# Kernel optimization log

Hardware: AMD Instinct MI355X
Metric: run time of the kernel (lower is better)

Reference implementation:

```python
import jax, jax.numpy as jnp
import numpy as np

ALPHA = 2000.0
TAU = 1e-07
K = 3
TOL = 1e-06
MAX_ITER = 50
T = 1048576  # 2**20
EPS = 1e-08


def setup_inputs() -> dict:
    key = jax.random.key(0)
    k1, k2 = jax.random.split(key)
    x = jax.random.normal(k1, (T,), dtype=jnp.float32)
    omega0 = jax.random.uniform(k2, (K,), dtype=jnp.float32)  # torch does 0.5*rand(K); scaled in reference
    return {"x": x, "omega0": omega0}


def _vmd(x, omega0):
    Tn = x.shape[0]
    freqs = jnp.arange(1, Tn + 1, dtype=jnp.float32) / Tn - 0.5 - 1.0 / Tn  # [T]
    f_hat = jnp.fft.fftshift(jnp.fft.fft(x.astype(jnp.complex64)))  # [T] complex64
    omega = 0.5 * omega0  # init == 1
    u0 = jnp.zeros((K, Tn), dtype=jnp.complex64)
    lam0 = jnp.zeros((Tn,), dtype=jnp.complex64)

    def step(carry, n):
        u_out, u_prev, lam_prev, om, done = carry
        # --- u_hat update (vectorized over k; torch k-loop uses stale omega) ---
        d_self = (freqs[None, :] - om[:, None]) ** 2            # [K,T]
        denom = d_self + TAU ** 2
        denom = denom.at[1:].add(d_self[:-1])                    # + (freqs - omega[k-1])^2 for k>0
        denom = denom.at[:-1].add(d_self[1:])                    # + (freqs - omega[k+1])^2 for k<K-1
        u_new = (f_hat[None, :] - lam_prev[None, :] / 2) / (1.0 + ALPHA * denom)  # [K,T]
        # --- omega update (DC == 0 branch) ---
        power = jnp.abs(u_new) ** 2                              # [K,T] float32
        om_new = jnp.sum(power * freqs[None, :], axis=1) / (jnp.sum(power, axis=1) + EPS)
        # --- dual ascent ---
        lam_new = lam_prev + TAU * (jnp.sum(u_new, axis=0) - f_hat)
        # --- convergence check every 10 outer iterations (torch break -> done flag) ---
        u_diff = jnp.sum(jnp.abs(u_new - u_prev) ** 2) / (jnp.sum(jnp.abs(u_prev) ** 2) + EPS)
        o_diff = jnp.sum(jnp.abs(om_new - jnp.roll(om_new, 1))) / K
        conv = (n % 10 == 0) & (u_diff < TOL) & (o_diff < TOL)
        new = (u_new, u_new, lam_new, om_new, done | conv)
        old = (u_out, u_prev, lam_prev, om, done)
        out = jax.tree_util.tree_map(lambda a, b: jnp.where(done, a, b), old, new)
        return out, None

    carry = (u0, u0, lam0, omega, jnp.array(False))
    (u_final, _, _, _, _), _ = jax.lax.scan(step, carry, jnp.arange(MAX_ITER))
    imfs = jnp.fft.ifft(jnp.fft.ifftshift(u_final, axes=1), axis=1).real.astype(x.dtype)  # [K,T]
    return imfs


def reference(x, omega0):
    return _vmd(x, omega0)
```

## Files before the change

### kernel.cpp

```cpp
#include <hip/hip_runtime.h>
#include <math.h>


#define TN        (1 << 20)
#define NBINS     1024
#define PPB       1024
#define FALPHA    2000.0f
#define FTAU      1e-7f
#define FTOL      1e-6f
#define FEPS      1e-8f
#define FTWO_PI   6.28318530717958647692f
#define FINV_T    (1.0f / 1048576.0f)

__device__ __forceinline__ float2 cmulf(float2 a, float2 b) {
    return make_float2(a.x * b.x - a.y * b.y, a.x * b.y + a.y * b.x);
}
__device__ __forceinline__ float2 cisf(float a) {
    float s, c;
    __sincosf(a, &s, &c);
    return make_float2(c, s);
}
__device__ __forceinline__ float rlanef(float v, int l) {
    return __int_as_float(__builtin_amdgcn_readlane(__float_as_int(v), l));
}

__device__ __forceinline__ void g3f(float fr, float om0, float om1, float om2,
                                    float& g0, float& g1, float& g2) {
    const float tau2 = FTAU * FTAU;
    float d0 = fr - om0; d0 *= d0;
    float d1 = fr - om1; d1 *= d1;
    float d2 = fr - om2; d2 *= d2;
    g0 = __builtin_amdgcn_rcpf(1.0f + FALPHA * (d0 + d1 + tau2));
    g1 = __builtin_amdgcn_rcpf(1.0f + FALPHA * (d0 + d1 + d2 + tau2));
    g2 = __builtin_amdgcn_rcpf(1.0f + FALPHA * (d1 + d2 + tau2));
}

__device__ __forceinline__ float dpp_wave_sum(float x) {
    x += __int_as_float(__builtin_amdgcn_update_dpp(
             0, __float_as_int(x), 0x111, 0xf, 0xf, true));
    x += __int_as_float(__builtin_amdgcn_update_dpp(
             0, __float_as_int(x), 0x112, 0xf, 0xf, true));
    x += __int_as_float(__builtin_amdgcn_update_dpp(
             0, __float_as_int(x), 0x114, 0xf, 0xf, true));
    x += __int_as_float(__builtin_amdgcn_update_dpp(
             0, __float_as_int(x), 0x118, 0xf, 0xf, true));
    x += __int_as_float(__builtin_amdgcn_update_dpp(
             0, __float_as_int(x), 0x142, 0xf, 0xf, true));
    x += __int_as_float(__builtin_amdgcn_update_dpp(
             0, __float_as_int(x), 0x143, 0xf, 0xf, true));
    return x;
}
__device__ __forceinline__ float dpp_sum32(float x) {
    x += __int_as_float(__builtin_amdgcn_update_dpp(
             0, __float_as_int(x), 0x111, 0xf, 0xf, true));
    x += __int_as_float(__builtin_amdgcn_update_dpp(
             0, __float_as_int(x), 0x112, 0xf, 0xf, true));
    x += __int_as_float(__builtin_amdgcn_update_dpp(
             0, __float_as_int(x), 0x114, 0xf, 0xf, true));
    x += __int_as_float(__builtin_amdgcn_update_dpp(
             0, __float_as_int(x), 0x118, 0xf, 0xf, true));
    x += __int_as_float(__builtin_amdgcn_update_dpp(
             0, __float_as_int(x), 0x142, 0xf, 0xf, true));
    return x;
}

__global__ __launch_bounds__(256)
void k_binpart(const float2* __restrict__ in, float* __restrict__ pB,
               float* __restrict__ pM) {
    __shared__ float tile[32][33];
    const int bx = blockIdx.x * 32, by = blockIdx.y * 32;
    const int tx = threadIdx.x, ty = threadIdx.y;
#pragma unroll
    for (int j = 0; j < 32; j += 8) {
        const float2 v = in[(size_t)(by + ty + j) * 1024 + bx + tx];
        tile[ty + j][tx] = v.x * v.x + v.y * v.y;
    }
    __syncthreads();
    const int sIdx = blockIdx.y;
    const float d = ((float)(by + tx) - 511.5f) * FINV_T;
    const int lane = (tx + 32 * ty) & 63;
#pragma unroll
    for (int j = 0; j < 32; j += 8) {
        float s = tile[tx][ty + j];
        float m = s * d;
        s = dpp_sum32(s);
        m = dpp_sum32(m);
        if (lane == 31 || lane == 63) {
            const int bin = bx + ty + j;
            pB[bin * 32 + sIdx] = s;
            pM[bin * 32 + sIdx] = m;
        }
    }
}

__global__ __launch_bounds__(256)
void k_omega(const float* __restrict__ pB, const float* __restrict__ pM,
             const float* __restrict__ omega0,
             float* __restrict__ oomf, float* __restrict__ sgsb) {
    const int tid = threadIdx.x;
    const int lane = tid & 63, wid = tid >> 6;
    const float kA = -4.0f * FALPHA;

    float B[4], M[4], C[4], SG[4], gp[4];
    const float4* __restrict__ pB4 = (const float4*)pB;
    const float4* __restrict__ pM4 = (const float4*)pM;
#pragma unroll
    for (int i = 0; i < 4; ++i) {
        const int j = tid + 256 * i;
        float sb = 0.f, sm = 0.f;
#pragma unroll
        for (int s = 0; s < 8; ++s) {
            const float4 b = pB4[j * 8 + s];
            sb += b.x; sb += b.y; sb += b.z; sb += b.w;
            const float4 m = pM4[j * 8 + s];
            sm += m.x; sm += m.y; sm += m.z; sm += m.w;
        }
        B[i] = sb; M[i] = sm;
        C[i] = ((float)(j * PPB) + 511.5f) * FINV_T - 0.5f;
        SG[i] = 0.f; gp[i] = 0.f;
    }

    float om0 = 0.5f * omega0[0];
    float om1 = 0.5f * omega0[1];
    float om2 = 0.5f * omega0[2];
    float op0 = om0, op1 = om1, op2 = om2;
    float n0 = om0, n1 = om1, n2 = om2;
    float stop = 0.f;

    __shared__ float wsum[2][4][8];
    bool fin = true;

    for (int n = 0; n < 49; ++n) {
        if (n > 0) {
            if (stop != 0.f) { fin = false; break; }
            op0 = om0; op1 = om1; op2 = om2;
            om0 = n0; om1 = n1; om2 = n2;
#pragma unroll
            for (int i = 0; i < 4; ++i) SG[i] += gp[i] - 1.0f;
        }
        const int check = (n > 0 && n % 10 == 0);

        float a[8];
#pragma unroll
        for (int v = 0; v < 8; ++v) a[v] = 0.f;

#pragma unroll
        for (int i = 0; i < 4; ++i) {
            const float c  = C[i];
            const float Bv = B[i];
            const float M1 = M[i];
            const float e0 = c - om0, e1 = c - om1, e2 = c - om2;
            float g0, g1, g2;
            g3f(c, om0, om1, om2, g0, g1, g2);
            const float gsq0 = g0 * g0, gsq1 = g1 * g1, gsq2 = g2 * g2;
            const float gc0 = gsq0 * g0, gc1 = gsq1 * g1, gc2 = gsq2 * g2;
            const float Dp0 = e0 + e1, Dp1 = e0 + e1 + e2, Dp2 = e1 + e2;
            const float P0 = gsq0 * Bv + kA * Dp0 * gc0 * M1;
            const float P1 = gsq1 * Bv + kA * Dp1 * gc1 * M1;
            const float P2 = gsq2 * Bv + kA * Dp2 * gc2 * M1;
            a[0] += P0; a[1] += P1; a[2] += P2;
            a[3] += c * P0 + gsq0 * M1;
            a[4] += c * P1 + gsq1 * M1;
            a[5] += c * P2 + gsq2 * M1;
            gp[i] = g0 + g1 + g2;
            if (check) {
                float h0, h1, h2;
                g3f(c, op0, op1, op2, h0, h1, h2);
                const float d0 = g0 - h0, d1 = g1 - h1, d2 = g2 - h2;
                a[6] += Bv * (d0 * d0 + d1 * d1 + d2 * d2);
                a[7] += Bv * (h0 * h0 + h1 * h1 + h2 * h2);
            }
        }
#pragma unroll
        for (int v = 0; v < 6; ++v) a[v] = dpp_wave_sum(a[v]);
        if (check) {
            a[6] = dpp_wave_sum(a[6]);
            a[7] = dpp_wave_sum(a[7]);
        }
        if (lane == 63) {
            *(float4*)&wsum[n & 1][wid][0] = make_float4(a[0], a[1], a[2], a[3]);
            *(float4*)&wsum[n & 1][wid][4] = make_float4(a[4], a[5], a[6], a[7]);
        }
        __syncthreads();
        float r = 0.f;
#pragma unroll
        for (int w = 0; w < 4; ++w) r += wsum[n & 1][w][lane & 7];
        const float S0 = rlanef(r, 0), S1 = rlanef(r, 1), S2 = rlanef(r, 2);
        const float S3 = rlanef(r, 3), S4 = rlanef(r, 4), S5 = rlanef(r, 5);
        n0 = S3 * __builtin_amdgcn_rcpf(S0 + FEPS);
        n1 = S4 * __builtin_amdgcn_rcpf(S1 + FEPS);
        n2 = S5 * __builtin_amdgcn_rcpf(S2 + FEPS);
        if (check) {
            const float S6 = rlanef(r, 6), S7 = rlanef(r, 7);
            const float ud = S6 * __builtin_amdgcn_rcpf(S7 + FEPS);
            const float od = (fabsf(n0 - n2) + fabsf(n1 - n0) +
                              fabsf(n2 - n1)) * (1.0f / 3.0f);
            stop = (ud < FTOL && od < FTOL) ? 1.f : 0.f;
        }
    }

    if (fin) {
#pragma unroll
        for (int i = 0; i < 4; ++i) SG[i] += gp[i] - 1.0f;
        om0 = n0; om1 = n1; om2 = n2;
    }
#pragma unroll
    for (int i = 0; i < 4; ++i) sgsb[tid + 256 * i] = SG[i];
    if (tid == 0) { oomf[0] = om0; oomf[1] = om1; oomf[2] = om2; }
}

__device__ __forceinline__ float2* fft1024_stages(float2* bufA, float2* bufB,
                                                  int t, float dir) {
    float2* src = bufA;
    float2* dst = bufB;
    int Ns = 1;
#pragma unroll
    for (int s = 0; s < 5; ++s) {
        const int jm = t & (Ns - 1);
        float2 v0 = src[t], v1 = src[t + 256], v2 = src[t + 512], v3 = src[t + 768];
        const float a = dir * (FTWO_PI * 0.25f) * ((float)jm / (float)Ns);
        float2 w1 = cisf(a);
        float2 w2 = cmulf(w1, w1);
        float2 w3 = cmulf(w2, w1);
        v1 = cmulf(v1, w1); v2 = cmulf(v2, w2); v3 = cmulf(v3, w3);
        float2 s0 = make_float2(v0.x + v2.x, v0.y + v2.y);
        float2 s1 = make_float2(v0.x - v2.x, v0.y - v2.y);
        float2 s2 = make_float2(v1.x + v3.x, v1.y + v3.y);
        float2 s3 = make_float2(v1.x - v3.x, v1.y - v3.y);
        float2 s3i = make_float2(-dir * s3.y, dir * s3.x);
        const int base = ((t - jm) << 2) + jm;
        dst[base]          = make_float2(s0.x + s2.x, s0.y + s2.y);
        dst[base + Ns]     = make_float2(s1.x + s3i.x, s1.y + s3i.y);
        dst[base + 2 * Ns] = make_float2(s0.x - s2.x, s0.y - s2.y);
        dst[base + 3 * Ns] = make_float2(s1.x - s3i.x, s1.y - s3i.y);
        __syncthreads();
        float2* tmp = src; src = dst; dst = tmp;
        Ns <<= 2;
    }
    return src;
}

__global__ __launch_bounds__(256)
void k_fft1024(const float2* __restrict__ in, float2* __restrict__ out,
               float dir, int do_tw) {
    __shared__ float2 bufA[1024];
    __shared__ float2 bufB[1024];
    const int row  = blockIdx.x;
    const int rowm = row & 1023;
    const float2* __restrict__ rin  = in  + (size_t)row * 1024;
    float2* __restrict__ rout = out + (size_t)row * 1024;
    const int t = threadIdx.x;
#pragma unroll
    for (int r = 0; r < 4; ++r) bufA[t + 256 * r] = rin[t + 256 * r];
    __syncthreads();
    float2* src = fft1024_stages(bufA, bufB, t, dir);
#pragma unroll
    for (int r = 0; r < 4; ++r) {
        const int c = t + 256 * r;
        float2 xv = src[c];
        if (do_tw) {
            const unsigned p = ((unsigned)rowm * (unsigned)c) & 1048575u;
            xv = cmulf(xv, cisf(dir * (FTWO_PI * FINV_T) * (float)p));
        }
        rout[c] = xv;
    }
}

__global__ __launch_bounds__(256)
void k_fftu(const float2* __restrict__ fhat, const float* __restrict__ sgsb,
            const float* __restrict__ oomf,
            float2* __restrict__ out, int zbase) {
    __shared__ float2 bufA[1024];
    __shared__ float2 bufB[1024];
    const int row = blockIdx.x & 1023;
    const int zi  = blockIdx.x >> 10;
    const int z   = zi + zbase;
    const float om0 = oomf[0], om1 = oomf[1], om2 = oomf[2];
    const float2* __restrict__ frow = fhat + (size_t)row * 1024;
    const int t = threadIdx.x;
#pragma unroll
    for (int r = 0; r < 4; ++r) {
        const int c = t + 256 * r;
        const float2 f = frow[c];
        const int tt = (c << 10) | row;
        const float fr = (float)tt * FINV_T - 0.5f;
        const float sc = 1.0f - 0.5f * FTAU * sgsb[tt >> 10];
        float g0, g1, g2;
        g3f(fr, om0, om1, om2, g0, g1, g2);
        const int tm = (TN - tt) & (TN - 1);
        const float frm = (float)tm * FINV_T - 0.5f;
        const float scm = 1.0f - 0.5f * FTAU * sgsb[tm >> 10];
        float h0, h1, h2;
        g3f(frm, om0, om1, om2, h0, h1, h2);
        float A, Bi;
        if (z == 0) {
            A  = 0.5f * (g0 * sc + h0 * scm);
            Bi = 0.5f * (g1 * sc + h1 * scm);
        } else {
            A  = 0.5f * (g2 * sc + h2 * scm);
            Bi = 0.f;
        }
        bufA[c] = cmulf(f, make_float2(A, Bi));
    }
    __syncthreads();
    float2* src = fft1024_stages(bufA, bufB, t, 1.0f);
    float2* __restrict__ rout = out + (size_t)zi * TN + (size_t)row * 1024;
#pragma unroll
    for (int r = 0; r < 4; ++r) {
        const int c = t + 256 * r;
        const unsigned p = ((unsigned)row * (unsigned)c) & 1048575u;
        rout[c] = cmulf(src[c], cisf((FTWO_PI * FINV_T) * (float)p));
    }
}

__global__ __launch_bounds__(256)
void k_fftu2(const float2* __restrict__ fhat, const float* __restrict__ sgsb,
             const float* __restrict__ oomf, float2* __restrict__ out) {
    __shared__ float2 bufA[1024];
    __shared__ float2 bufB[1024];
    const int row = blockIdx.x;
    const float om0 = oomf[0], om1 = oomf[1], om2 = oomf[2];
    const float2* __restrict__ frow = fhat + (size_t)row * 1024;
    const int t = threadIdx.x;
    float2 fsave[4];
    float  A2s[4];
    float2 tws[4];
#pragma unroll
    for (int r = 0; r < 4; ++r) {
        const int c = t + 256 * r;
        const float2 f = frow[c];
        const int tt = (c << 10) | row;
        const float fr = (float)tt * FINV_T - 0.5f;
        const float sc = 1.0f - 0.5f * FTAU * sgsb[tt >> 10];
        float g0, g1, g2;
        g3f(fr, om0, om1, om2, g0, g1, g2);
        const int tm = (TN - tt) & (TN - 1);
        const float frm = (float)tm * FINV_T - 0.5f;
        const float scm = 1.0f - 0.5f * FTAU * sgsb[tm >> 10];
        float h0, h1, h2;
        g3f(frm, om0, om1, om2, h0, h1, h2);
        const float A  = 0.5f * (g0 * sc + h0 * scm);
        const float Bi = 0.5f * (g1 * sc + h1 * scm);
        A2s[r]   = 0.5f * (g2 * sc + h2 * scm);
        fsave[r] = f;
        bufA[c] = cmulf(f, make_float2(A, Bi));
    }
    __syncthreads();
    float2* src = fft1024_stages(bufA, bufB, t, 1.0f);
    float2* __restrict__ r0 = out + (size_t)row * 1024;
#pragma unroll
    for (int r = 0; r < 4; ++r) {
        const int c = t + 256 * r;
        const unsigned p = ((unsigned)row * (unsigned)c) & 1048575u;
        tws[r] = cisf((FTWO_PI * FINV_T) * (float)p);
        r0[c] = cmulf(src[c], tws[r]);
    }
#pragma unroll
    for (int r = 0; r < 4; ++r) {
        const int c = t + 256 * r;
        bufA[c] = cmulf(fsave[r], make_float2(A2s[r], 0.f));
    }
    __syncthreads();
    src = fft1024_stages(bufA, bufB, t, 1.0f);
    float2* __restrict__ r1 = out + (size_t)TN + (size_t)row * 1024;
#pragma unroll
    for (int r = 0; r < 4; ++r) {
        const int c = t + 256 * r;
        r1[c] = cmulf(src[c], tws[r]);
    }
}

__global__ __launch_bounds__(256)
void k_tr_c2c(const float2* __restrict__ in, float2* __restrict__ out) {
    __shared__ float2 tile[32][33];
    const size_t zo = (size_t)blockIdx.z * TN;
    const int bx = blockIdx.x * 32, by = blockIdx.y * 32;
    const int tx = threadIdx.x, ty = threadIdx.y;
#pragma unroll
    for (int j = 0; j < 32; j += 8)
        tile[ty + j][tx] = in[zo + (size_t)(by + ty + j) * 1024 + bx + tx];
    __syncthreads();
#pragma unroll
    for (int j = 0; j < 32; j += 8)
        out[zo + (size_t)(bx + ty + j) * 1024 + by + tx] = tile[tx][ty + j];
}

__global__ __launch_bounds__(256)
void k_tr_fwd_in(const float* __restrict__ in, float2* __restrict__ out) {
    __shared__ float tile[32][33];
    const int bx = blockIdx.x * 32, by = blockIdx.y * 32;
    const int tx = threadIdx.x, ty = threadIdx.y;
#pragma unroll
    for (int j = 0; j < 32; j += 8)
        tile[ty + j][tx] = in[(size_t)(by + ty + j) * 1024 + bx + tx];
    __syncthreads();
#pragma unroll
    for (int j = 0; j < 32; j += 8) {
        const int r = bx + ty + j;
        float v = tile[tx][ty + j];
        v = (r & 1) ? -v : v;
        out[(size_t)r * 1024 + by + tx] = make_float2(v, 0.0f);
    }
}

__global__ __launch_bounds__(256)
void k_tr_out(const float2* __restrict__ in, float* __restrict__ out,
              int zbase) {
    __shared__ float2 tile[32][33];
    const int z = blockIdx.z + zbase;
    const size_t zo = (size_t)blockIdx.z * TN;
    const int bx = blockIdx.x * 32, by = blockIdx.y * 32;
    const int tx = threadIdx.x, ty = threadIdx.y;
#pragma unroll
    for (int j = 0; j < 32; j += 8)
        tile[ty + j][tx] = in[zo + (size_t)(by + ty + j) * 1024 + bx + tx];
    __syncthreads();
    const int c = by + tx;
    const float sgn = (c & 1) ? -FINV_T : FINV_T;
#pragma unroll
    for (int j = 0; j < 32; j += 8) {
        const int r = bx + ty + j;
        const float2 v = tile[tx][ty + j];
        const size_t idx = (size_t)r * 1024 + c;
        if (z == 0) {
            out[idx]              = v.x * sgn;
            out[(size_t)TN + idx] = v.y * sgn;
        } else {
            out[2 * (size_t)TN + idx] = v.x * sgn;
        }
    }
}

extern "C" void kernel_launch(void* const* d_in, const int* in_sizes, int n_in,
                              void* d_out, int out_size, void* d_ws, size_t ws_size,
                              hipStream_t stream) {
    (void)in_sizes; (void)n_in; (void)out_size;
    const float* x      = (const float*)d_in[0];
    const float* omega0 = (const float*)d_in[1];
    float* outp = (float*)d_out;
    char* ws = (char*)d_ws;

    const size_t MB = (size_t)1 << 20;
    const size_t KB = (size_t)1 << 10;
    float2* fhat = (float2*)(ws);
    float*  pB   = (float*)(ws + 8 * MB);
    float*  pM   = (float*)(ws + 8 * MB + 128 * KB);
    float*  sgsb = (float*)(ws + 8 * MB + 256 * KB);
    float*  oomf = (float*)(ws + 8 * MB + 264 * KB);
    const bool batch2 = ws_size >= 42 * MB;
    float2* sA = (float2*)(ws + 9 * MB);
    float2* sB = batch2 ? (float2*)(ws + 25 * MB)
                        : (float2*)(ws + 17 * MB);

    dim3 tb(32, 8);
    dim3 tg(32, 32);

    k_tr_fwd_in<<<tg, tb, 0, stream>>>(x, sA);
    k_fft1024<<<1024, 256, 0, stream>>>(sA, sB, -1.0f, 1);
    k_tr_c2c<<<tg, tb, 0, stream>>>(sB, sA);
    k_fft1024<<<1024, 256, 0, stream>>>(sA, fhat, -1.0f, 0);

    k_binpart<<<tg, tb, 0, stream>>>(fhat, pB, pM);

    k_omega<<<1, 256, 0, stream>>>(pB, pM, omega0, oomf, sgsb);

    if (batch2) {
        k_fftu2<<<1024, 256, 0, stream>>>(fhat, sgsb, oomf, sB);
        k_tr_c2c<<<dim3(32, 32, 2), tb, 0, stream>>>(sB, sA);
        k_fft1024<<<2048, 256, 0, stream>>>(sA, sB, 1.0f, 0);
        k_tr_out<<<dim3(32, 32, 2), tb, 0, stream>>>(sB, outp, 0);
    } else {
        for (int z = 0; z < 2; ++z) {
            k_fftu<<<1024, 256, 0, stream>>>(fhat, sgsb, oomf, sB, z);
            k_tr_c2c<<<tg, tb, 0, stream>>>(sB, sA);
            k_fft1024<<<1024, 256, 0, stream>>>(sA, sB, 1.0f, 0);
            k_tr_out<<<dim3(32, 32, 1), tb, 0, stream>>>(sB, outp, z);
        }
    }
}
```

Before: 178.5 us.

## Fuse transposes into column-slab FFT kernels for forward and inverse passes

```diff
diff --git a/kernel.cpp b/kernel.cpp
--- a/kernel.cpp
+++ b/kernel.cpp
@@ -240,6 +240,42 @@
     return src;
 }
 
+__device__ __forceinline__ float2* fft1024_stages4(float2* bufA, float2* bufB,
+                                                   int t, float dir) {
+    float2* src = bufA;
+    float2* dst = bufB;
+    int Ns = 1;
+#pragma unroll
+    for (int s = 0; s < 5; ++s) {
+        const int jm = t & (Ns - 1);
+        const float a = dir * (FTWO_PI * 0.25f) * ((float)jm / (float)Ns);
+        float2 w1 = cisf(a);
+        float2 w2 = cmulf(w1, w1);
+        float2 w3 = cmulf(w2, w1);
+        const int base = ((t - jm) << 2) + jm;
+#pragma unroll
+        for (int q = 0; q < 4; ++q) {
+            const int o = q * 1024;
+            float2 v0 = src[o + t],       v1 = src[o + t + 256];
+            float2 v2 = src[o + t + 512], v3 = src[o + t + 768];
+            v1 = cmulf(v1, w1); v2 = cmulf(v2, w2); v3 = cmulf(v3, w3);
+            float2 s0 = make_float2(v0.x + v2.x, v0.y + v2.y);
+            float2 s1 = make_float2(v0.x - v2.x, v0.y - v2.y);
+            float2 s2 = make_float2(v1.x + v3.x, v1.y + v3.y);
+            float2 s3 = make_float2(v1.x - v3.x, v1.y - v3.y);
+            float2 s3i = make_float2(-dir * s3.y, dir * s3.x);
+            dst[o + base]          = make_float2(s0.x + s2.x, s0.y + s2.y);
+            dst[o + base + Ns]     = make_float2(s1.x + s3i.x, s1.y + s3i.y);
+            dst[o + base + 2 * Ns] = make_float2(s0.x - s2.x, s0.y - s2.y);
+            dst[o + base + 3 * Ns] = make_float2(s1.x - s3i.x, s1.y - s3i.y);
+        }
+        __syncthreads();
+        float2* tmp = src; src = dst; dst = tmp;
+        Ns <<= 2;
+    }
+    return src;
+}
+
 __global__ __launch_bounds__(256)
 void k_fft1024(const float2* __restrict__ in, float2* __restrict__ out,
                float dir, int do_tw) {
@@ -263,6 +299,85 @@
             xv = cmulf(xv, cisf(dir * (FTWO_PI * FINV_T) * (float)p));
         }
         rout[c] = xv;
+    }
+}
+
+__global__ __launch_bounds__(256)
+void k_fftfwd_slab(const float* __restrict__ x, float2* __restrict__ sA) {
+    __shared__ float2 bufA[4][1024];
+    __shared__ float2 bufB[4][1024];
+    const int a0 = blockIdx.x * 4;
+    const int t  = threadIdx.x;
+#pragma unroll
+    for (int r = 0; r < 4; ++r) {
+        const int p = t + 256 * r;
+        const float4 v = *(const float4*)(x + (size_t)p * 1024 + a0);
+        bufA[0][p] = make_float2( v.x, 0.f);
+        bufA[1][p] = make_float2(-v.y, 0.f);
+        bufA[2][p] = make_float2( v.z, 0.f);
+        bufA[3][p] = make_float2(-v.w, 0.f);
+    }
+    __syncthreads();
+    float2* src = fft1024_stages4(&bufA[0][0], &bufB[0][0], t, -1.0f);
+#pragma unroll
+    for (int r = 0; r < 4; ++r) {
+        const int c = t + 256 * r;
+        float2 o[4];
+#pragma unroll
+        for (int q = 0; q < 4; ++q) {
+            const unsigned p = ((unsigned)(a0 + q) * (unsigned)c) & 1048575u;
+            o[q] = cmulf(src[q * 1024 + c],
+                         cisf(-(FTWO_PI * FINV_T) * (float)p));
+        }
+        float2* w = sA + (size_t)c * 1024 + a0;
+        *(float4*)(w)     = make_float4(o[0].x, o[0].y, o[1].x, o[1].y);
+        *(float4*)(w + 2) = make_float4(o[2].x, o[2].y, o[3].x, o[3].y);
+    }
+}
+
+__global__ __launch_bounds__(256)
+void k_ifft_slab(const float2* __restrict__ zin, float* __restrict__ out,
+                 int zbase) {
+    __shared__ float2 bufA[4][1024];
+    __shared__ float2 bufB[4][1024];
+    const int m0 = blockIdx.x * 4;
+    const int zi = blockIdx.y;
+    const int z  = zi + zbase;
+    const int t  = threadIdx.x;
+    const float2* __restrict__ Z = zin + (size_t)zi * TN;
+#pragma unroll
+    for (int r = 0; r < 4; ++r) {
+        const int k = t + 256 * r;
+        const float4 u0 = *(const float4*)(Z + (size_t)k * 1024 + m0);
+        const float4 u1 = *(const float4*)(Z + (size_t)k * 1024 + m0 + 2);
+        bufA[0][k] = make_float2(u0.x, u0.y);
+        bufA[1][k] = make_float2(u0.z, u0.w);
+        bufA[2][k] = make_float2(u1.x, u1.y);
+        bufA[3][k] = make_float2(u1.z, u1.w);
+    }
+    __syncthreads();
+    float2* src = fft1024_stages4(&bufA[0][0], &bufB[0][0], t, 1.0f);
+#pragma unroll
+    for (int r = 0; r < 4; ++r) {
+        const int m2 = t + 256 * r;
+        float re[4], im[4];
+#pragma unroll
+        for (int q = 0; q < 4; ++q) {
+            const float sgn = (q & 1) ? -FINV_T : FINV_T;
+            const float2 v = src[q * 1024 + m2];
+            re[q] = v.x * sgn;
+            im[q] = v.y * sgn;
+        }
+        const size_t idx = (size_t)m2 * 1024 + m0;
+        if (z == 0) {
+            *(float4*)(out + idx) =
+                make_float4(re[0], re[1], re[2], re[3]);
+            *(float4*)(out + (size_t)TN + idx) =
+                make_float4(im[0], im[1], im[2], im[3]);
+        } else {
+            *(float4*)(out + 2 * (size_t)TN + idx) =
+                make_float4(re[0], re[1], re[2], re[3]);
+        }
     }
 }
 
@@ -370,67 +485,6 @@
     }
 }
 
-__global__ __launch_bounds__(256)
-void k_tr_c2c(const float2* __restrict__ in, float2* __restrict__ out) {
-    __shared__ float2 tile[32][33];
-    const size_t zo = (size_t)blockIdx.z * TN;
-    const int bx = blockIdx.x * 32, by = blockIdx.y * 32;
-    const int tx = threadIdx.x, ty = threadIdx.y;
-#pragma unroll
-    for (int j = 0; j < 32; j += 8)
-        tile[ty + j][tx] = in[zo + (size_t)(by + ty + j) * 1024 + bx + tx];
-    __syncthreads();
-#pragma unroll
-    for (int j = 0; j < 32; j += 8)
-        out[zo + (size_t)(bx + ty + j) * 1024 + by + tx] = tile[tx][ty + j];
-}
-
-__global__ __launch_bounds__(256)
-void k_tr_fwd_in(const float* __restrict__ in, float2* __restrict__ out) {
-    __shared__ float tile[32][33];
-    const int bx = blockIdx.x * 32, by = blockIdx.y * 32;
-    const int tx = threadIdx.x, ty = threadIdx.y;
-#pragma unroll
-    for (int j = 0; j < 32; j += 8)
-        tile[ty + j][tx] = in[(size_t)(by + ty + j) * 1024 + bx + tx];
-    __syncthreads();
-#pragma unroll
-    for (int j = 0; j < 32; j += 8) {
-        const int r = bx + ty + j;
-        float v = tile[tx][ty + j];
-        v = (r & 1) ? -v : v;
-        out[(size_t)r * 1024 + by + tx] = make_float2(v, 0.0f);
-    }
-}
-
-__global__ __launch_bounds__(256)
-void k_tr_out(const float2* __restrict__ in, float* __restrict__ out,
-              int zbase) {
-    __shared__ float2 tile[32][33];
-    const int z = blockIdx.z + zbase;
-    const size_t zo = (size_t)blockIdx.z * TN;
-    const int bx = blockIdx.x * 32, by = blockIdx.y * 32;
-    const int tx = threadIdx.x, ty = threadIdx.y;
-#pragma unroll
-    for (int j = 0; j < 32; j += 8)
-        tile[ty + j][tx] = in[zo + (size_t)(by + ty + j) * 1024 + bx + tx];
-    __syncthreads();
-    const int c = by + tx;
-    const float sgn = (c & 1) ? -FINV_T : FINV_T;
-#pragma unroll
-    for (int j = 0; j < 32; j += 8) {
-        const int r = bx + ty + j;
-        const float2 v = tile[tx][ty + j];
-        const size_t idx = (size_t)r * 1024 + c;
-        if (z == 0) {
-            out[idx]              = v.x * sgn;
-            out[(size_t)TN + idx] = v.y * sgn;
-        } else {
-            out[2 * (size_t)TN + idx] = v.x * sgn;
-        }
-    }
-}
-
 extern "C" void kernel_launch(void* const* d_in, const int* in_sizes, int n_in,
                               void* d_out, int out_size, void* d_ws, size_t ws_size,
                               hipStream_t stream) {
@@ -452,29 +506,20 @@
     float2* sB = batch2 ? (float2*)(ws + 25 * MB)
                         : (float2*)(ws + 17 * MB);
 
-    dim3 tb(32, 8);
-    dim3 tg(32, 32);
-
-    k_tr_fwd_in<<<tg, tb, 0, stream>>>(x, sA);
-    k_fft1024<<<1024, 256, 0, stream>>>(sA, sB, -1.0f, 1);
-    k_tr_c2c<<<tg, tb, 0, stream>>>(sB, sA);
+    k_fftfwd_slab<<<256, 256, 0, stream>>>(x, sA);
     k_fft1024<<<1024, 256, 0, stream>>>(sA, fhat, -1.0f, 0);
 
-    k_binpart<<<tg, tb, 0, stream>>>(fhat, pB, pM);
+    k_binpart<<<dim3(32, 32), dim3(32, 8), 0, stream>>>(fhat, pB, pM);
 
     k_omega<<<1, 256, 0, stream>>>(pB, pM, omega0, oomf, sgsb);
 
     if (batch2) {
         k_fftu2<<<1024, 256, 0, stream>>>(fhat, sgsb, oomf, sB);
-        k_tr_c2c<<<dim3(32, 32, 2), tb, 0, stream>>>(sB, sA);
-        k_fft1024<<<2048, 256, 0, stream>>>(sA, sB, 1.0f, 0);
-        k_tr_out<<<dim3(32, 32, 2), tb, 0, stream>>>(sB, outp, 0);
+        k_ifft_slab<<<dim3(256, 2), 256, 0, stream>>>(sB, outp, 0);
     } else {
         for (int z = 0; z < 2; ++z) {
             k_fftu<<<1024, 256, 0, stream>>>(fhat, sgsb, oomf, sB, z);
-            k_tr_c2c<<<tg, tb, 0, stream>>>(sB, sA);
-            k_fft1024<<<1024, 256, 0, stream>>>(sA, sB, 1.0f, 0);
-            k_tr_out<<<dim3(32, 32, 1), tb, 0, stream>>>(sB, outp, z);
-        }
-    }
-}
+            k_ifft_slab<<<dim3(256, 1), 256, 0, stream>>>(sB, outp, z);
+        }
+    }
+}
```

Measured after the change: 166.1 us. -7.0%, faster.
